# Kernel tuning notes

Hardware: AMD Instinct MI355X
Metric: run time of the kernel (lower is better)

Reference implementation:

```python
import jax, jax.numpy as jnp
import numpy as np

B = 2
C = 256
NA = 3  # aspect ratios per location
IMG_H, IMG_W = 800, 1216
FEAT_SHAPES = [(200, 304), (100, 152), (50, 76), (25, 38), (13, 19)]
STRIDES = [4, 8, 16, 32, 64]
SIZES = [32, 64, 128, 256, 512]
RATIOS = np.array([0.5, 1.0, 2.0])
PRE_NMS = 1000
POST_NMS = 1000
NMS_TH = 0.7
MIN_SIZE = 1e-3
BBOX_CLIP = float(np.log(1000.0 / 16.0))
NUM_PER_LEVEL = [h * w * NA for h, w in FEAT_SHAPES]


def _make_anchors():
    out = []
    for (h, w), stride, size in zip(FEAT_SHAPES, STRIDES, SIZES):
        hr = np.sqrt(RATIOS)
        wr = 1.0 / hr
        ws, hs = wr * size, hr * size
        base = np.stack([-ws / 2, -hs / 2, ws / 2, hs / 2], 1)  # [NA,4]
        yy, xx = np.meshgrid(np.arange(h) * stride, np.arange(w) * stride, indexing='ij')
        shifts = np.stack([xx.ravel(), yy.ravel(), xx.ravel(), yy.ravel()], 1)  # [h*w,4]
        out.append((shifts[:, None, :] + base[None, :, :]).reshape(-1, 4))
    return jnp.asarray(np.concatenate(out, 0), jnp.float32)  # [A,4]

ANCHORS = _make_anchors()
# level id of each selected (per-level top-k) anchor is static
LEVELS_SEL = jnp.asarray(
    np.concatenate([np.full(min(PRE_NMS, a), i) for i, a in enumerate(NUM_PER_LEVEL)]),
    jnp.float32)


def conv2d(x, w, b, pad):
    y = jax.lax.conv_general_dilated(x, w, (1, 1), [(pad, pad), (pad, pad)],
                                     dimension_numbers=('NCHW', 'OIHW', 'NCHW'))
    return y + b[None, :, None, None]


def decode(reg, anc):
    # BoxCoder.decode with weights (1,1,1,1)
    wa = anc[..., 2] - anc[..., 0]
    ha = anc[..., 3] - anc[..., 1]
    cxa = anc[..., 0] + 0.5 * wa
    cya = anc[..., 1] + 0.5 * ha
    dx, dy = reg[..., 0], reg[..., 1]
    dw = jnp.minimum(reg[..., 2], BBOX_CLIP)
    dh = jnp.minimum(reg[..., 3], BBOX_CLIP)
    cx = dx * wa + cxa
    cy = dy * ha + cya
    w = jnp.exp(dw) * wa
    h = jnp.exp(dh) * ha
    return jnp.stack([cx - 0.5 * w, cy - 0.5 * h, cx + 0.5 * w, cy + 0.5 * h], -1)


def _nms_select(boxes, scores, valid, lvl_offsets):
    # batched_nms via per-level coordinate offset trick; greedy NMS over IoU matrix
    b = boxes + lvl_offsets[:, None]
    s = jnp.where(valid, scores, -jnp.inf)
    order = jnp.argsort(-s)
    bs = b[order]
    keep = valid[order]
    area = (bs[:, 2] - bs[:, 0]) * (bs[:, 3] - bs[:, 1])
    lt = jnp.maximum(bs[:, None, :2], bs[None, :, :2])
    rb = jnp.minimum(bs[:, None, 2:], bs[None, :, 2:])
    wh = jnp.clip(rb - lt, 0.0)
    inter = wh[..., 0] * wh[..., 1]
    iou = inter / (area[:, None] + area[None, :] - inter + 1e-9)
    K = boxes.shape[0]
    ar = jnp.arange(K)

    def body(i, keep):
        sup = keep[i] & (iou[i] > NMS_TH) & (ar > i)
        return keep & ~sup

    keep = jax.lax.fori_loop(0, K, body, keep)
    keep_orig = jnp.zeros(K, bool).at[order].set(keep)
    ms = jnp.where(keep_orig, scores, -jnp.inf)
    top_s, idx = jax.lax.top_k(ms, POST_NMS)
    return idx, jnp.isfinite(top_s)


def reference(feat0, feat1, feat2, feat3, feat4, conv_w, conv_b, cls_w, cls_b, box_w, box_b):
    logit_l, reg_l = [], []
    for f in (feat0, feat1, feat2, feat3, feat4):
        t = jax.nn.relu(conv2d(f, conv_w, conv_b, 1))
        l = conv2d(t, cls_w, cls_b, 0)   # [B,NA,H,W]
        r = conv2d(t, box_w, box_b, 0)   # [B,NA*4,H,W]
        _, _, H, W = l.shape
        logit_l.append(l.transpose(0, 2, 3, 1).reshape(B, -1))                        # HWC order
        reg_l.append(r.reshape(B, NA, 4, H, W).transpose(0, 3, 4, 1, 2).reshape(B, -1, 4))
    logits = jnp.concatenate(logit_l, 1)   # [B,A]
    regs = jnp.concatenate(reg_l, 1)       # [B,A,4]
    proposals = decode(regs, ANCHORS[None])  # [B,A,4]

    # per-level top-k (pre-NMS)
    sel, off = [], 0
    for a in NUM_PER_LEVEL:
        k = min(PRE_NMS, a)
        _, idx = jax.lax.top_k(logits[:, off:off + a], k)
        sel.append(idx + off)
        off += a
    sel = jnp.concatenate(sel, 1)          # [B,Ksel]
    bi = jnp.arange(B)[:, None]
    sc = logits[bi, sel]
    bx = proposals[bi, sel]

    # clip to image, remove small boxes (mask)
    x0 = jnp.clip(bx[..., 0], 0.0, float(IMG_W))
    y0 = jnp.clip(bx[..., 1], 0.0, float(IMG_H))
    x1 = jnp.clip(bx[..., 2], 0.0, float(IMG_W))
    y1 = jnp.clip(bx[..., 3], 0.0, float(IMG_H))
    bx = jnp.stack([x0, y0, x1, y1], -1)
    valid = ((x1 - x0) >= MIN_SIZE) & ((y1 - y0) >= MIN_SIZE)
    offs = LEVELS_SEL * (float(max(IMG_W, IMG_H)) + 1.0)

    idx2, vout = jax.vmap(lambda b_, s_, v_: _nms_select(b_, s_, v_, offs))(
        jax.lax.stop_gradient(bx), jax.lax.stop_gradient(sc), valid)

    boxes_out = jnp.take_along_axis(bx, idx2[..., None], 1)   # [B,POST_NMS,4]
    scores_out = jnp.take_along_axis(sc, idx2, 1)             # [B,POST_NMS]
    boxes_out = jnp.where(vout[..., None], boxes_out, 0.0)
    scores_out = jnp.where(vout, scores_out, -1e9)
    return boxes_out, scores_out


def setup_inputs() -> dict:
    key = jax.random.key(0)
    ks = jax.random.split(key, 9)
    inp = {}
    for i, (h, w) in enumerate(FEAT_SHAPES):
        inp[f'feat{i}'] = jax.random.normal(ks[i], (B, C, h, w), jnp.float32)
    inp['conv_w'] = jax.random.normal(ks[5], (C, C, 3, 3), jnp.float32) * 0.01
    inp['conv_b'] = jnp.zeros((C,), jnp.float32)
    inp['cls_w'] = jax.random.normal(ks[6], (NA, C, 1, 1), jnp.float32) * 0.01
    inp['cls_b'] = jnp.zeros((NA,), jnp.float32)
    inp['box_w'] = jax.random.normal(ks[7], (NA * 4, C, 1, 1), jnp.float32) * 0.01
    inp['box_b'] = jnp.zeros((NA * 4,), jnp.float32)
    return inp
```

## Files before the change

kernel.cpp:

```cpp
#include <hip/hip_runtime.h>
#include <hip/hip_fp16.h>
#include <stdint.h>
#include <math.h>

typedef unsigned int uint;
typedef unsigned short ushort;
typedef unsigned long long ull;
typedef __attribute__((ext_vector_type(8))) _Float16 f16x8;
typedef __attribute__((ext_vector_type(4))) float f32x4;

#define BATCH 2
#define ATOTAL 242991
#define KSEL 4741
#define NW 75
#define POST_NMS 1000
#define WB_ELEMS (72*2*2*8*64*8)

__device__ __constant__ int dLoff[5]  = {0,182400,228000,239400,242250};
__device__ __constant__ int dCount[5] = {182400,45600,11400,2850,741};
__device__ __constant__ int dSeg[5]   = {0,1000,2000,3000,4000};
__device__ __constant__ int dSegK[5]  = {1000,1000,1000,1000,741};
__device__ __constant__ int dHc[5]     = {200,100,50,25,13};
__device__ __constant__ int dWc[5]     = {304,152,76,38,19};
__device__ __constant__ int dTilesX[5] = {19,10,5,3,2};
__device__ __constant__ int dCumT[6]   = {0,475,605,640,652,656};
__device__ __constant__ int dStrideC[5]= {4,8,16,32,64};
__device__ __constant__ int dSizeC[5]  = {32,64,128,256,512};

__device__ __forceinline__ uint fkey(float f) {
    uint u = __float_as_uint(f);
    return (u & 0x80000000u) ? ~u : (u | 0x80000000u);
}
__device__ __forceinline__ ushort h2u(__half h) {
    union { __half h; ushort u; } x; x.h = h; return x.u;
}

__global__ __launch_bounds__(256) void wt_kernel(const float* __restrict__ conv_w,
                                                 ushort* __restrict__ wB) {
    int t = blockIdx.x * 256 + threadIdx.x;
    if (t >= WB_ELEMS) return;
    int e    = t & 7;
    int lane = (t >> 3) & 63;
    int nt   = (t >> 9) & 7;
    int r12  = t >> 12;
    int pl   = r12 & 1;
    int r2   = r12 >> 1;
    int ocg  = r2 & 1;
    int step = r2 >> 1;
    int icblk = step / 9, dydx = step - icblk * 9;
    int oc = ocg * 128 + nt * 16 + (lane & 15);
    int ic = icblk * 32 + ((lane >> 4) << 3) + e;
    float v = conv_w[(size_t)oc * 2304 + ic * 9 + dydx];
    __half h = __float2half(v);
    float r = (v - __half2float(h)) * 1024.0f;
    __half m = __float2half(r);
    wB[t] = (pl == 0) ? h2u(h) : h2u(m);
}

__global__ __launch_bounds__(512) void conv_mfma_all(
    const float* __restrict__ f0, const float* __restrict__ f1,
    const float* __restrict__ f2, const float* __restrict__ f3,
    const float* __restrict__ f4, const ushort* __restrict__ wB,
    const float* __restrict__ conv_b,
    const float* __restrict__ cls_w, const float* __restrict__ cls_b,
    const float* __restrict__ box_w, const float* __restrict__ box_b,
    float* __restrict__ scoresA, float* __restrict__ boxesA)
{
    const int bidx = blockIdx.x;
    const int b    = blockIdx.y;
    const int tid  = threadIdx.x;

    int lvl = 0;
#pragma unroll
    for (int l = 1; l < 5; ++l) if (bidx >= dCumT[l]) lvl = l;
    const int tile   = bidx - dCumT[lvl];
    const int H      = dHc[lvl], W = dWc[lvl];
    const int TILESX = dTilesX[lvl];
    const int ty0    = (tile / TILESX) * 8;
    const int tx0    = (tile % TILESX) * 16;
    const int HW     = H * W;
    const float* feat = (lvl == 0) ? f0 : (lvl == 1) ? f1 : (lvl == 2) ? f2 : (lvl == 3) ? f3 : f4;
    const float* fb = feat + (size_t)b * 256 * HW;

    __shared__ __align__(16) char uni[39424];
    ushort* halo = (ushort*)uni;
    ushort* ldsB = (ushort*)(uni + 23040);
    float*  tS   = (float*)uni;
    float*  hw2  = (float*)(uni + 32768);
    double* houtD= (double*)uni;

    const int lane = tid & 63, wave = tid >> 6;
    const int wm = wave >> 1, wn = wave & 1;
    const int g = lane >> 4, col = lane & 15;
    const int laneA = g * 1440 + col * 8;

    int  hdst[12]; int hoff[12]; bool hval[12];
#pragma unroll
    for (int j = 0; j < 12; ++j) {
        int e = tid + j * 512;
        hdst[j] = -1; hoff[j] = 0; hval[j] = false;
        if (e < 5760) {
            int ic = e / 180, rem = e - ic * 180;
            int hrow = rem / 18, hcol = rem - hrow * 18;
            int gy = ty0 + hrow - 1, gx = tx0 + hcol - 1;
            hdst[j] = (((ic >> 3) * 10 + hrow) * 18 + hcol) * 8 + (ic & 7);
            if (gy >= 0 && gy < H && gx >= 0 && gx < W) {
                hval[j] = true; hoff[j] = ic * HW + gy * W + gx;
            }
        }
    }

    double hacc[4] = {0,0,0,0};

    uint4 Br0, Br1;
    {
        const uint4* gq = (const uint4*)wB;
        Br0 = gq[tid]; Br1 = gq[tid + 512];
    }

#pragma unroll 1
    for (int ocg = 0; ocg < 2; ++ocg) {
        f32x4 accH[2][4], accM[2][4];
#pragma unroll
        for (int mi = 0; mi < 2; ++mi)
#pragma unroll
            for (int ni = 0; ni < 4; ++ni) {
                accH[mi][ni] = (f32x4){0.f, 0.f, 0.f, 0.f};
                accM[mi][ni] = (f32x4){0.f, 0.f, 0.f, 0.f};
            }

#pragma unroll 1
        for (int s = 0; s < 72; ++s) {
            const int icblk = s / 9;
            const int dydx  = s - icblk * 9;
            const int dy = dydx / 3, dx = dydx - dy * 3;

            __syncthreads();
            if (dydx == 0) {
                float hv[12];
                const float* fcb = fb + (size_t)icblk * 32 * HW;
#pragma unroll
                for (int j = 0; j < 12; ++j)
                    hv[j] = hval[j] ? fcb[hoff[j]] : 0.f;
#pragma unroll
                for (int j = 0; j < 12; ++j) {
                    if (hdst[j] >= 0) {
                        float v = hv[j];
                        __half h = __float2half(v);
                        float r = (v - __half2float(h)) * 1024.0f;
                        __half m = __float2half(r);
                        int li = hdst[j];
                        halo[li] = h2u(h); halo[5760 + li] = h2u(m);
                    }
                }
            }
            {
                uint4* lq = (uint4*)ldsB;
                lq[tid] = Br0; lq[tid + 512] = Br1;
            }
            __syncthreads();
            {
                int gstep = ocg * 72 + s + 1;
                if (gstep < 144) {
                    int s2 = gstep % 72, og2 = gstep / 72;
                    const uint4* gq = (const uint4*)(wB + ((size_t)(s2 * 2 + og2)) * 8192);
                    Br0 = gq[tid]; Br1 = gq[tid + 512];
                }
            }
            f16x8 Ah[2], Am[2];
            const int abase = laneA + dx * 8 + (2 * wm + dy) * 144;
#pragma unroll
            for (int mi = 0; mi < 2; ++mi) {
                Ah[mi] = *(const f16x8*)(halo + abase + mi * 144);
                Am[mi] = *(const f16x8*)(halo + 5760 + abase + mi * 144);
            }
#pragma unroll
            for (int ni = 0; ni < 4; ++ni) {
                const int nt = 4 * wn + ni;
                f16x8 Bh = *(const f16x8*)(ldsB + ((0 * 8 + nt) * 64 + lane) * 8);
                f16x8 Bm = *(const f16x8*)(ldsB + ((1 * 8 + nt) * 64 + lane) * 8);
#pragma unroll
                for (int mi = 0; mi < 2; ++mi) {
                    f32x4 cH = accH[mi][ni];
                    f32x4 cM = accM[mi][ni];
                    cH = __builtin_amdgcn_mfma_f32_16x16x32_f16(Ah[mi], Bh, cH, 0, 0, 0);
                    cM = __builtin_amdgcn_mfma_f32_16x16x32_f16(Ah[mi], Bm, cM, 0, 0, 0);
                    cM = __builtin_amdgcn_mfma_f32_16x16x32_f16(Am[mi], Bh, cM, 0, 0, 0);
                    accH[mi][ni] = cH;
                    accM[mi][ni] = cM;
                }
            }
        }
        __syncthreads();
        float cb[4];
#pragma unroll
        for (int ni = 0; ni < 4; ++ni)
            cb[ni] = conv_b[ocg * 128 + (4 * wn + ni) * 16 + col];

#pragma unroll 1
        for (int s2 = 0; s2 < 2; ++s2) {
            if (wn == s2) {
#pragma unroll
                for (int mi = 0; mi < 2; ++mi) {
#pragma unroll
                    for (int r = 0; r < 4; ++r) {
                        int px = (2 * wm + mi) * 16 + 4 * g + r;
                        int sw = px & 15;
#pragma unroll
                        for (int ni = 0; ni < 4; ++ni) {
                            int slot = (ni * 4 + (col >> 2)) ^ sw;
                            float val = accH[mi][ni][r] + accM[mi][ni][r] * 0.0009765625f;
                            tS[px * 64 + slot * 4 + (col & 3)] =
                                fmaxf(val + cb[ni], 0.f);
                        }
                    }
                }
            }
            if (tid < 256) {
                const int oc2 = tid >> 2;
                const int h0  = (tid & 3) * 4;
                const int oc  = ocg * 128 + s2 * 64 + oc2;
                float vv[4];
#pragma unroll
                for (int q = 0; q < 4; ++q) {
                    int h = h0 + q;
                    vv[q] = (h < 3) ? cls_w[h * 256 + oc]
                          : (h < 15) ? box_w[(h - 3) * 256 + oc] : 0.f;
                }
                *(float4*)&hw2[oc2 * 16 + h0] = make_float4(vv[0], vv[1], vv[2], vv[3]);
            }
            __syncthreads();
            {
                const int px = tid & 127;
                const int hh = tid >> 7;
                const int sw = px & 15;
#pragma unroll 1
                for (int j4 = 0; j4 < 16; ++j4) {
                    float4 t4 = *(const float4*)&tS[px * 64 + (j4 ^ sw) * 4];
                    float tv[4] = {t4.x, t4.y, t4.z, t4.w};
#pragma unroll
                    for (int jj = 0; jj < 4; ++jj) {
                        const float* hb = &hw2[(j4 * 4 + jj) * 16 + hh * 4];
                        float4 h0 = *(const float4*)hb;
                        double tv_d = (double)tv[jj];
                        hacc[0] += tv_d * (double)h0.x;
                        hacc[1] += tv_d * (double)h0.y;
                        hacc[2] += tv_d * (double)h0.z;
                        hacc[3] += tv_d * (double)h0.w;
                    }
                }
            }
            __syncthreads();
        }
    }

    {
        const int px = tid & 127;
        const int hh = tid >> 7;
#pragma unroll
        for (int j = 0; j < 4; ++j) houtD[px * 16 + hh * 4 + j] = hacc[j];
    }
    __syncthreads();

    if (tid < 128) {
        const int px = tid;
        const int gy = ty0 + (px >> 4);
        const int gx = tx0 + (px & 15);
        if (gy < H && gx < W) {
            const int STRIDE = dStrideC[lvl];
            const int SZ     = dSizeC[lvl];
            const int LOFF   = dLoff[lvl];
#pragma unroll 1
            for (int a = 0; a < 3; ++a) {
                double score = houtD[px * 16 + a] + (double)cls_b[a];
                double rg0 = houtD[px * 16 + 3 + a * 4 + 0] + (double)box_b[a * 4 + 0];
                double rg1 = houtD[px * 16 + 3 + a * 4 + 1] + (double)box_b[a * 4 + 1];
                double rg2 = houtD[px * 16 + 3 + a * 4 + 2] + (double)box_b[a * 4 + 2];
                double rg3 = houtD[px * 16 + 3 + a * 4 + 3] + (double)box_b[a * 4 + 3];
                double ratio = (a == 0) ? 0.5 : ((a == 1) ? 1.0 : 2.0);
                double hr = sqrt(ratio), wr = 1.0 / hr;
                double wsd = wr * (double)SZ, hsd = hr * (double)SZ;
                double sx = (double)(gx * STRIDE), sy = (double)(gy * STRIDE);
                float ax0 = (float)(sx - 0.5 * wsd);
                float ay0 = (float)(sy - 0.5 * hsd);
                float ax1 = (float)(sx + 0.5 * wsd);
                float ay1 = (float)(sy + 0.5 * hsd);
                double wa = (double)ax1 - (double)ax0, ha = (double)ay1 - (double)ay0;
                double cxa = (double)ax0 + 0.5 * wa, cya = (double)ay0 + 0.5 * ha;
                double dwv = fmin(rg2, 4.135166556742356);
                double dhv = fmin(rg3, 4.135166556742356);
                double cx = rg0 * wa + cxa, cy = rg1 * ha + cya;
                double w = exp(dwv) * wa, h = exp(dhv) * ha;
                double x0 = cx - 0.5 * w, y0 = cy - 0.5 * h;
                double x1 = cx + 0.5 * w, y1 = cy + 0.5 * h;
                x0 = fmin(fmax(x0, 0.0), 1216.0);
                y0 = fmin(fmax(y0, 0.0), 800.0);
                x1 = fmin(fmax(x1, 0.0), 1216.0);
                y1 = fmin(fmax(y1, 0.0), 800.0);
                int gidx = LOFF + (gy * W + gx) * 3 + a;
                scoresA[(size_t)b * ATOTAL + gidx] = (float)score;
                float4 bx = make_float4((float)x0, (float)y0, (float)x1, (float)y1);
                *(float4*)&boxesA[((size_t)b * ATOTAL + gidx) * 4] = bx;
            }
        }
    }
}

__global__ __launch_bounds__(1024) void topk_kernel(
    const float* __restrict__ scoresA, const float* __restrict__ boxesA,
    float* __restrict__ selScore, float* __restrict__ selBox,
    int* __restrict__ selValid, int* __restrict__ selAnchor)
{
    const int lvl = blockIdx.x, b = blockIdx.y;
    const int n = dCount[lvl], loff = dLoff[lvl], seg = dSeg[lvl], k = dSegK[lvl];
    const float* sc = scoresA + (size_t)b * ATOTAL + loff;
    const int tid = threadIdx.x;

    float* oS = selScore + b * KSEL;
    float* oB = selBox + (size_t)b * KSEL * 4;
    int* oV = selValid + b * KSEL;
    int* oA = selAnchor + b * KSEL;

    auto emit = [&](int slot, int i) {
        int g = loff + i;
        float s = sc[i];
        float4 bx = *(const float4*)&boxesA[((size_t)b * ATOTAL + g) * 4];
        oS[seg + slot] = s;
        *(float4*)&oB[(size_t)(seg + slot) * 4] = bx;
        oV[seg + slot] = ((bx.z - bx.x) >= 1e-3f && (bx.w - bx.y) >= 1e-3f) ? 1 : 0;
        oA[seg + slot] = g;
    };

    if (n <= k) {
        for (int i = tid; i < n; i += 1024) emit(i, i);
        return;
    }

    __shared__ uint hist[2048];
    __shared__ uint sh_bin, sh_krem;
    __shared__ uint cntG, cntE;
    __shared__ int stash[64];

    uint krem = (uint)k;
    uint prefix = 0;
    for (int pass = 0; pass < 3; ++pass) {
        for (int e = tid; e < 2048; e += 1024) hist[e] = 0;
        __syncthreads();
        for (int i = tid; i < n; i += 1024) {
            uint key = fkey(sc[i]);
            uint bin; bool sel;
            if (pass == 0)      { sel = true;                      bin = key >> 21; }
            else if (pass == 1) { sel = ((key >> 21) == prefix);   bin = (key >> 10) & 0x7FFu; }
            else                { sel = ((key >> 10) == prefix);   bin = key & 0x3FFu; }
            if (sel) atomicAdd(&hist[bin], 1u);
        }
        __syncthreads();
        if (tid == 0) {
            int nb = (pass == 2) ? 1024 : 2048;
            uint c = 0;
            for (int x = nb - 1; x >= 0; --x) {
                uint h = hist[x];
                if (c + h >= krem) { sh_bin = (uint)x; sh_krem = krem - c; break; }
                c += h;
            }
        }
        __syncthreads();
        uint bin = sh_bin; krem = sh_krem;
        if (pass == 0)      prefix = bin;
        else if (pass == 1) prefix = (prefix << 11) | bin;
        else                prefix = (prefix << 10) | bin;
        __syncthreads();
    }
    const uint T = prefix;
    const uint need_eq = krem;
    if (tid == 0) { cntG = 0; cntE = 0; }
    __syncthreads();
    for (int i = tid; i < n; i += 1024) {
        uint key = fkey(sc[i]);
        if (key > T) {
            uint pos = atomicAdd(&cntG, 1u);
            emit((int)pos, i);
        } else if (key == T) {
            uint e = atomicAdd(&cntE, 1u);
            if (e < 64) stash[e] = i;
        }
    }
    __syncthreads();
    if (tid == 0) {
        uint ne = cntE < 64u ? cntE : 64u;
        uint base = cntG;
        for (uint t2 = 0; t2 < need_eq; ++t2) {
            int best = -1, bj = -1;
            for (uint j2 = 0; j2 < ne; ++j2) {
                int v = stash[j2];
                if (v >= 0 && (best < 0 || v < best)) { best = v; bj = j2; }
            }
            if (bj >= 0) { stash[bj] = -1; emit((int)(base + t2), best); }
            else emit((int)(base + t2), 0);
        }
    }
}

__global__ __launch_bounds__(1024) void sort_kernel(
    const float* __restrict__ selScore, const float* __restrict__ selBox,
    const int* __restrict__ selValid, const int* __restrict__ selAnchor,
    int* __restrict__ sortedSlot, float* __restrict__ sortedBoxOff,
    ull* __restrict__ validMask)
{
    const int b = blockIdx.x, tid = threadIdx.x;
    __shared__ ull  skey[8192];
    __shared__ uint spay[8192];
    __shared__ ull  svm[NW];

    for (int i = tid; i < 8192; i += 1024) {
        ull kk2; uint pp;
        if (i < KSEL) {
            float s = selScore[b * KSEL + i];
            int v = selValid[b * KSEL + i];
            uint k32 = v ? fkey(s) : 0x007FFFFFu;
            uint a32 = 0xFFFFFFFFu - (uint)selAnchor[b * KSEL + i];
            kk2 = ((ull)k32 << 32) | a32; pp = (uint)i;
        } else { kk2 = 0ull; pp = 0xFFFFFFFFu; }
        skey[i] = kk2; spay[i] = pp;
    }
    __syncthreads();
    for (uint kk = 2; kk <= 8192; kk <<= 1) {
        for (uint j = kk >> 1; j > 0; j >>= 1) {
            for (int i = tid; i < 8192; i += 1024) {
                uint ixj = (uint)i ^ j;
                if (ixj > (uint)i) {
                    bool up = ((((uint)i) & kk) == 0);
                    ull a = skey[i], c = skey[ixj];
                    bool sw = up ? (a < c) : (a > c);
                    if (sw) {
                        skey[i] = c; skey[ixj] = a;
                        uint tp = spay[i]; spay[i] = spay[ixj]; spay[ixj] = tp;
                    }
                }
            }
            __syncthreads();
        }
    }
    for (int i = tid; i < NW; i += 1024) svm[i] = 0ull;
    __syncthreads();
    for (int i = tid; i < KSEL; i += 1024) {
        uint slot = spay[i];
        sortedSlot[b * KSEL + i] = (int)slot;
        int v = selValid[b * KSEL + slot];
        if (v) atomicOr(&svm[i >> 6], 1ull << (i & 63));
        int lvl = (int)slot / 1000;
        float off = 1217.0f * (float)lvl;
        float4 bx = *(const float4*)&selBox[((size_t)b * KSEL + slot) * 4];
        bx.x += off; bx.y += off; bx.z += off; bx.w += off;
        *(float4*)&sortedBoxOff[((size_t)b * KSEL + i) * 4] = bx;
    }
    __syncthreads();
    for (int i = tid; i < NW; i += 1024) validMask[b * NW + i] = svm[i];
}

__global__ __launch_bounds__(64) void nms_mask(const float* __restrict__ sortedBoxOff,
                                               ull* __restrict__ mat)
{
    const int jb = blockIdx.x, ib = blockIdx.y, b = blockIdx.z;
    const int tid = threadIdx.x;
    __shared__ float4 bj[64];
    __shared__ float  aj[64];
    const int j0 = jb * 64;
    const int jn = (KSEL - j0) < 64 ? (KSEL - j0) : 64;
    if (tid < jn) {
        float4 v = *(const float4*)&sortedBoxOff[((size_t)b * KSEL + j0 + tid) * 4];
        bj[tid] = v; aj[tid] = (v.z - v.x) * (v.w - v.y);
    }
    __syncthreads();
    const int i = ib * 64 + tid;
    if (i >= KSEL) return;
    float4 bi = *(const float4*)&sortedBoxOff[((size_t)b * KSEL + i) * 4];
    float ai = (bi.z - bi.x) * (bi.w - bi.y);
    ull m = 0ull;
    for (int jj = 0; jj < jn; ++jj) {
        int j = j0 + jj;
        if (j <= i) continue;
        float4 bb = bj[jj];
        float ltx = fmaxf(bi.x, bb.x), lty = fmaxf(bi.y, bb.y);
        float rbx = fminf(bi.z, bb.z), rby = fminf(bi.w, bb.w);
        float wx = fmaxf(rbx - ltx, 0.f), wy = fmaxf(rby - lty, 0.f);
        float inter = wx * wy;
        float iou = inter / (ai + aj[jj] - inter + 1e-9f);
        if (iou > 0.7f) m |= (1ull << jj);
    }
    mat[((size_t)b * KSEL + i) * NW + jb] = m;
}

#define LOADG(RA, RB, G) { int base0 = (G) * 16; \
    _Pragma("unroll") for (int d = 0; d < 16; ++d) { int i = base0 + d; \
        RA[d] = (i < KSEL) ? mb[(size_t)i * NW + lane] : 0ull; \
        RB[d] = (hasHi && i < KSEL) ? mb[(size_t)i * NW + 64 + lane] : 0ull; } }
#define PROCG(RA, RB, G) { int base0 = (G) * 16; \
    _Pragma("unroll") for (int d = 0; d < 16; ++d) { int i = base0 + d; \
        if (i < KSEL) { int wi = i >> 6; \
            ull act0 = v0 & ~s0, act1 = v1 & ~s1; \
            ull aw = (wi < 64) ? __shfl(act0, wi, 64) : __shfl(act1, wi - 64, 64); \
            if ((aw >> (i & 63)) & 1ull) { \
                s0 |= RA[d]; s1 |= RB[d]; \
                if (lane == 0) keptPos[b * POST_NMS + nk] = i; \
                ++nk; \
                if (nk == POST_NMS) { if (lane == 0) nkOut[b] = nk; return; } } } } }

__global__ __launch_bounds__(64) void nms_scan(const ull* __restrict__ mat,
                                               const ull* __restrict__ validMask,
                                               int* __restrict__ keptPos,
                                               int* __restrict__ nkOut)
{
    const int b = blockIdx.x, lane = threadIdx.x;
    const bool hasHi = lane < NW - 64;
    ull v0 = validMask[b * NW + lane];
    ull v1 = hasHi ? validMask[b * NW + 64 + lane] : 0ull;
    ull s0 = 0ull, s1 = 0ull;
    int nk = 0;
    const ull* mb = mat + (size_t)b * KSEL * NW;
    const int NG = (KSEL + 15) / 16;

    ull A0[16], B0[16], A1[16], B1[16];
    LOADG(A0, B0, 0);
    for (int g = 0; g < NG; g += 2) {
        if (g + 1 < NG) LOADG(A1, B1, g + 1);
        PROCG(A0, B0, g);
        if (g + 2 < NG) LOADG(A0, B0, g + 2);
        if (g + 1 < NG) PROCG(A1, B1, g + 1);
    }
    if (lane == 0) nkOut[b] = nk;
}

__global__ __launch_bounds__(256) void out_kernel(
    const int* __restrict__ keptPos, const int* __restrict__ nkOut,
    const int* __restrict__ sortedSlot,
    const float* __restrict__ selBox, const float* __restrict__ selScore,
    float* __restrict__ out)
{
    int t = blockIdx.x * 256 + threadIdx.x;
    if (t >= BATCH * POST_NMS) return;
    int b = t / POST_NMS, row = t - b * POST_NMS;
    float4 bx = make_float4(0.f, 0.f, 0.f, 0.f);
    float sc = -1e9f;
    if (row < nkOut[b]) {
        int i = keptPos[b * POST_NMS + row];
        int slot = sortedSlot[b * KSEL + i];
        bx = *(const float4*)&selBox[((size_t)b * KSEL + slot) * 4];
        sc = selScore[b * KSEL + slot];
    }
    *(float4*)&out[(size_t)t * 4] = bx;
    out[BATCH * POST_NMS * 4 + t] = sc;
}

extern "C" void kernel_launch(void* const* d_in, const int* in_sizes, int n_in,
                              void* d_out, int out_size, void* d_ws, size_t ws_size,
                              hipStream_t stream)
{
    (void)in_sizes; (void)n_in; (void)out_size; (void)ws_size;
    const float* feat[5] = {(const float*)d_in[0], (const float*)d_in[1],
                            (const float*)d_in[2], (const float*)d_in[3],
                            (const float*)d_in[4]};
    const float* conv_w = (const float*)d_in[5];
    const float* conv_b = (const float*)d_in[6];
    const float* cls_w  = (const float*)d_in[7];
    const float* cls_b  = (const float*)d_in[8];
    const float* box_w  = (const float*)d_in[9];
    const float* box_b  = (const float*)d_in[10];
    float* out = (float*)d_out;

    char* ws = (char*)d_ws;
    size_t off = 0;
    auto carve = [&](size_t bytes) -> void* {
        void* p = (void*)(ws + off);
        off += (bytes + 255) & ~(size_t)255;
        return p;
    };
    ushort* wB         = (ushort*)carve((size_t)WB_ELEMS * 2);
    float* scoresA     = (float*)carve((size_t)BATCH * ATOTAL * 4);
    float* boxesA      = (float*)carve((size_t)BATCH * ATOTAL * 16);
    float* selScore    = (float*)carve((size_t)BATCH * KSEL * 4);
    float* selBox      = (float*)carve((size_t)BATCH * KSEL * 16);
    int*   selValid    = (int*)  carve((size_t)BATCH * KSEL * 4);
    int*   selAnchor   = (int*)  carve((size_t)BATCH * KSEL * 4);
    int*   sortedSlot  = (int*)  carve((size_t)BATCH * KSEL * 4);
    float* sortedBoxOff= (float*)carve((size_t)BATCH * KSEL * 16);
    ull*   validMask   = (ull*)  carve((size_t)BATCH * NW * 8);
    ull*   mat         = (ull*)  carve((size_t)BATCH * KSEL * NW * 8);
    int*   keptPos     = (int*)  carve((size_t)BATCH * POST_NMS * 4);
    int*   nkOut       = (int*)  carve(64);

    wt_kernel<<<(WB_ELEMS + 255) / 256, 256, 0, stream>>>(conv_w, wB);

    conv_mfma_all<<<dim3(656, BATCH), 512, 0, stream>>>(
        feat[0], feat[1], feat[2], feat[3], feat[4], wB, conv_b,
        cls_w, cls_b, box_w, box_b, scoresA, boxesA);

    topk_kernel<<<dim3(5, BATCH), 1024, 0, stream>>>(scoresA, boxesA, selScore, selBox, selValid, selAnchor);
    sort_kernel<<<dim3(BATCH), 1024, 0, stream>>>(selScore, selBox, selValid, selAnchor, sortedSlot, sortedBoxOff, validMask);
    nms_mask<<<dim3(NW, NW, BATCH), 64, 0, stream>>>(sortedBoxOff, mat);
    nms_scan<<<dim3(BATCH), 64, 0, stream>>>(mat, validMask, keptPos, nkOut);
    out_kernel<<<dim3((BATCH * POST_NMS + 255) / 256), 256, 0, stream>>>(keptPos, nkOut, sortedSlot, selBox, selScore, out);
}
```

Baseline: 1.598 ms.

## Stage three dx taps of weights per sync and launch only upper-triangle NMS blocks

The conv weight staging now covers all three dx taps of a (icblk, dy) row per step. This cuts the main loop from 72 to 24 synchronised steps per output-channel group, with three MFMA sub-steps per sync, and raises the LDS footprint and register-held prefetch buffers from two to six uint4. The NMS mask kernel launches only the upper-triangular block pairs (2850 instead of 75x75) and decodes the pair index in a loop. The scan masks out lower-triangle words it no longer computes. The larger LDS and register use may reduce occupancy in the conv kernel.

```diff
diff --git a/kernel.cpp b/kernel.cpp
--- a/kernel.cpp
+++ b/kernel.cpp
@@ -14,7 +14,8 @@
 #define KSEL 4741
 #define NW 75
 #define POST_NMS 1000
-#define WB_ELEMS (72*2*2*8*64*8)
+#define WB_ELEMS (2*8*3*3*2*8*64*8)
+#define NPAIRS 2850
 
 __device__ __constant__ int dLoff[5]  = {0,182400,228000,239400,242250};
 __device__ __constant__ int dCount[5] = {182400,45600,11400,2850,741};
@@ -42,18 +43,18 @@
     int e    = t & 7;
     int lane = (t >> 3) & 63;
     int nt   = (t >> 9) & 7;
-    int r12  = t >> 12;
-    int pl   = r12 & 1;
-    int r2   = r12 >> 1;
-    int ocg  = r2 & 1;
-    int step = r2 >> 1;
-    int icblk = step / 9, dydx = step - icblk * 9;
+    int pl   = (t >> 12) & 1;
+    int r    = t >> 13;
+    int dx = r % 3; r /= 3;
+    int dy = r % 3; r /= 3;
+    int icblk = r & 7;
+    int ocg = r >> 3;
     int oc = ocg * 128 + nt * 16 + (lane & 15);
     int ic = icblk * 32 + ((lane >> 4) << 3) + e;
-    float v = conv_w[(size_t)oc * 2304 + ic * 9 + dydx];
+    float v = conv_w[(size_t)oc * 2304 + ic * 9 + dy * 3 + dx];
     __half h = __float2half(v);
-    float r = (v - __half2float(h)) * 1024.0f;
-    __half m = __float2half(r);
+    float rr = (v - __half2float(h)) * 1024.0f;
+    __half m = __float2half(rr);
     wB[t] = (pl == 0) ? h2u(h) : h2u(m);
 }
 
@@ -82,7 +83,7 @@
     const float* feat = (lvl == 0) ? f0 : (lvl == 1) ? f1 : (lvl == 2) ? f2 : (lvl == 3) ? f3 : f4;
     const float* fb = feat + (size_t)b * 256 * HW;
 
-    __shared__ __align__(16) char uni[39424];
+    __shared__ __align__(16) char uni[72192];
     ushort* halo = (ushort*)uni;
     ushort* ldsB = (ushort*)(uni + 23040);
     float*  tS   = (float*)uni;
@@ -112,10 +113,12 @@
 
     double hacc[4] = {0,0,0,0};
 
-    uint4 Br0, Br1;
+    uint4 Br0, Br1, Br2, Br3, Br4, Br5;
     {
         const uint4* gq = (const uint4*)wB;
-        Br0 = gq[tid]; Br1 = gq[tid + 512];
+        Br0 = gq[tid];        Br1 = gq[tid + 512];
+        Br2 = gq[tid + 1024]; Br3 = gq[tid + 1536];
+        Br4 = gq[tid + 2048]; Br5 = gq[tid + 2560];
     }
 
 #pragma unroll 1
@@ -130,13 +133,12 @@
             }
 
 #pragma unroll 1
-        for (int s = 0; s < 72; ++s) {
-            const int icblk = s / 9;
-            const int dydx  = s - icblk * 9;
-            const int dy = dydx / 3, dx = dydx - dy * 3;
+        for (int s = 0; s < 24; ++s) {
+            const int icblk = s / 3;
+            const int dy    = s - icblk * 3;
 
             __syncthreads();
-            if (dydx == 0) {
+            if (dy == 0) {
                 float hv[12];
                 const float* fcb = fb + (size_t)icblk * 32 * HW;
 #pragma unroll
@@ -147,8 +149,8 @@
                     if (hdst[j] >= 0) {
                         float v = hv[j];
                         __half h = __float2half(v);
-                        float r = (v - __half2float(h)) * 1024.0f;
-                        __half m = __float2half(r);
+                        float rr = (v - __half2float(h)) * 1024.0f;
+                        __half m = __float2half(rr);
                         int li = hdst[j];
                         halo[li] = h2u(h); halo[5760 + li] = h2u(m);
                     }
@@ -156,38 +158,44 @@
             }
             {
                 uint4* lq = (uint4*)ldsB;
-                lq[tid] = Br0; lq[tid + 512] = Br1;
+                lq[tid] = Br0;         lq[tid + 512]  = Br1;
+                lq[tid + 1024] = Br2;  lq[tid + 1536] = Br3;
+                lq[tid + 2048] = Br4;  lq[tid + 2560] = Br5;
             }
             __syncthreads();
             {
-                int gstep = ocg * 72 + s + 1;
-                if (gstep < 144) {
-                    int s2 = gstep % 72, og2 = gstep / 72;
-                    const uint4* gq = (const uint4*)(wB + ((size_t)(s2 * 2 + og2)) * 8192);
-                    Br0 = gq[tid]; Br1 = gq[tid + 512];
-                }
-            }
-            f16x8 Ah[2], Am[2];
-            const int abase = laneA + dx * 8 + (2 * wm + dy) * 144;
-#pragma unroll
-            for (int mi = 0; mi < 2; ++mi) {
-                Ah[mi] = *(const f16x8*)(halo + abase + mi * 144);
-                Am[mi] = *(const f16x8*)(halo + 5760 + abase + mi * 144);
-            }
-#pragma unroll
-            for (int ni = 0; ni < 4; ++ni) {
-                const int nt = 4 * wn + ni;
-                f16x8 Bh = *(const f16x8*)(ldsB + ((0 * 8 + nt) * 64 + lane) * 8);
-                f16x8 Bm = *(const f16x8*)(ldsB + ((1 * 8 + nt) * 64 + lane) * 8);
+                int gstep = ocg * 24 + s + 1;
+                if (gstep < 48) {
+                    const uint4* gq = (const uint4*)(wB + (size_t)gstep * 24576);
+                    Br0 = gq[tid];        Br1 = gq[tid + 512];
+                    Br2 = gq[tid + 1024]; Br3 = gq[tid + 1536];
+                    Br4 = gq[tid + 2048]; Br5 = gq[tid + 2560];
+                }
+            }
+#pragma unroll 1
+            for (int dx = 0; dx < 3; ++dx) {
+                f16x8 Ah[2], Am[2];
+                const int abase = laneA + dx * 8 + (2 * wm + dy) * 144;
 #pragma unroll
                 for (int mi = 0; mi < 2; ++mi) {
-                    f32x4 cH = accH[mi][ni];
-                    f32x4 cM = accM[mi][ni];
-                    cH = __builtin_amdgcn_mfma_f32_16x16x32_f16(Ah[mi], Bh, cH, 0, 0, 0);
-                    cM = __builtin_amdgcn_mfma_f32_16x16x32_f16(Ah[mi], Bm, cM, 0, 0, 0);
-                    cM = __builtin_amdgcn_mfma_f32_16x16x32_f16(Am[mi], Bh, cM, 0, 0, 0);
-                    accH[mi][ni] = cH;
-                    accM[mi][ni] = cM;
+                    Ah[mi] = *(const f16x8*)(halo + abase + mi * 144);
+                    Am[mi] = *(const f16x8*)(halo + 5760 + abase + mi * 144);
+                }
+#pragma unroll
+                for (int ni = 0; ni < 4; ++ni) {
+                    const int nt = 4 * wn + ni;
+                    f16x8 Bh = *(const f16x8*)(ldsB + (size_t)(dx * 16 + nt) * 512 + lane * 8);
+                    f16x8 Bm = *(const f16x8*)(ldsB + (size_t)(dx * 16 + 8 + nt) * 512 + lane * 8);
+#pragma unroll
+                    for (int mi = 0; mi < 2; ++mi) {
+                        f32x4 cH = accH[mi][ni];
+                        f32x4 cM = accM[mi][ni];
+                        cH = __builtin_amdgcn_mfma_f32_16x16x32_f16(Ah[mi], Bh, cH, 0, 0, 0);
+                        cM = __builtin_amdgcn_mfma_f32_16x16x32_f16(Ah[mi], Bm, cM, 0, 0, 0);
+                        cM = __builtin_amdgcn_mfma_f32_16x16x32_f16(Am[mi], Bh, cM, 0, 0, 0);
+                        accH[mi][ni] = cH;
+                        accM[mi][ni] = cM;
+                    }
                 }
             }
         }
@@ -461,8 +469,12 @@
 __global__ __launch_bounds__(64) void nms_mask(const float* __restrict__ sortedBoxOff,
                                                ull* __restrict__ mat)
 {
-    const int jb = blockIdx.x, ib = blockIdx.y, b = blockIdx.z;
+    const int b = blockIdx.y;
     const int tid = threadIdx.x;
+    int rem = blockIdx.x, ib = 0;
+    while (rem >= NW - ib) { rem -= NW - ib; ++ib; }
+    const int jb = ib + rem;
+
     __shared__ float4 bj[64];
     __shared__ float  aj[64];
     const int j0 = jb * 64;
@@ -501,7 +513,8 @@
             ull act0 = v0 & ~s0, act1 = v1 & ~s1; \
             ull aw = (wi < 64) ? __shfl(act0, wi, 64) : __shfl(act1, wi - 64, 64); \
             if ((aw >> (i & 63)) & 1ull) { \
-                s0 |= RA[d]; s1 |= RB[d]; \
+                s0 |= (lane >= wi) ? RA[d] : 0ull; \
+                s1 |= (lane + 64 >= wi) ? RB[d] : 0ull; \
                 if (lane == 0) keptPos[b * POST_NMS + nk] = i; \
                 ++nk; \
                 if (nk == POST_NMS) { if (lane == 0) nkOut[b] = nk; return; } } } } }
@@ -597,7 +610,7 @@
 
     topk_kernel<<<dim3(5, BATCH), 1024, 0, stream>>>(scoresA, boxesA, selScore, selBox, selValid, selAnchor);
     sort_kernel<<<dim3(BATCH), 1024, 0, stream>>>(selScore, selBox, selValid, selAnchor, sortedSlot, sortedBoxOff, validMask);
-    nms_mask<<<dim3(NW, NW, BATCH), 64, 0, stream>>>(sortedBoxOff, mat);
+    nms_mask<<<dim3(NPAIRS, BATCH), 64, 0, stream>>>(sortedBoxOff, mat);
     nms_scan<<<dim3(BATCH), 64, 0, stream>>>(mat, validMask, keptPos, nkOut);
     out_kernel<<<dim3((BATCH * POST_NMS + 255) / 256), 256, 0, stream>>>(keptPos, nkOut, sortedSlot, selBox, selScore, out);
 }
```

Result: faster. 1.527 ms (-4.4%).
